# Performance work log

Measured on AMD Instinct MI355X. Metric: run time of the kernel, lower is better.

## Reference

```python
import jax, jax.numpy as jnp
from jax import lax
import numpy as np

CLASS_NUMBER = 19
REGION_RADIUS = 1
KERNEL = 2 * REGION_RADIUS + 1  # 3
IMAGE_TOPK = 256
EPS = 1e-6


def setup_inputs() -> dict:
    key = jax.random.key(0)
    # softmax-like probabilities over classes
    raw = jax.random.uniform(key, (4, CLASS_NUMBER, 512, 1024), dtype=jnp.float32)
    logit = raw / jnp.sum(raw, axis=1, keepdims=True)
    return {"logit": logit}


def _box_sum(x):
    # kxk box sum with zero padding (SAME for odd kernel == pad=radius)
    return lax.reduce_window(x, jnp.float32(0), lax.add,
                             (1, 1, KERNEL, KERNEL), (1, 1, 1, 1), 'SAME')


def reference(logit):
    B, C, H, W = logit.shape
    logC = jnp.log(jnp.float32(C))

    # region uncertainty: normalized entropy, then avg-pool (count_include_pad)
    entropy = jnp.sum(-logit * jnp.log(logit + EPS), axis=1, keepdims=True) / logC
    region_uncertainty = _box_sum(entropy) / (KERNEL * KERNEL)  # [B,1,H,W]

    # region impurity: argmax -> one-hot -> depthwise box-sum (ones kernel)
    predict = jnp.argmax(logit, axis=1)                       # [B,H,W]
    one_hot = jax.nn.one_hot(predict, C, axis=1, dtype=logit.dtype)  # [B,C,H,W]
    summary = _box_sum(one_hot)                               # [B,C,H,W]
    count = jnp.sum(summary, axis=1, keepdims=True)           # [B,1,H,W]
    dist = summary / count
    region_impurity = jnp.sum(-dist * jnp.log(dist + EPS), axis=1, keepdims=True) / logC

    score = region_uncertainty * region_impurity              # [B,1,H,W]

    # per-image score: sum of top-k region scores
    flat = score.reshape(B, H * W)
    topk_vals, _ = lax.top_k(flat, IMAGE_TOPK)
    image_score = jnp.sum(topk_vals, axis=1)                  # [B]
    return image_score
```

## Files before the change

### kernel.cpp

```cpp
#include <hip/hip_runtime.h>
#include <cstdint>
#include <cstddef>

#define BB 4
#define CC 19
#define HH 512
#define WW 1024
#define HW (HH*WW)
#define HW4 (HW/4)
#define BHW (BB*HW)
#define KTOP 256
#define EPSF 1e-6f
#define NB1 4096
#define NB2 8192
#define SEG 128
#define LSTRIDE 1032
#define LOGC 2.9444389791664403f

__device__ __forceinline__ unsigned int sortable(float x) {
    unsigned int u = __float_as_uint(x);
    return (u & 0x80000000u) ? ~u : (u | 0x80000000u);
}
__device__ __forceinline__ float unsortable(unsigned int K) {
    unsigned int u = (K & 0x80000000u) ? (K & 0x7FFFFFFFu) : ~K;
    return __uint_as_float(u);
}

__global__ __launch_bounds__(256) void k_ent(const float4* __restrict__ logit,
                                             float4* __restrict__ ent,
                                             uchar4* __restrict__ pred,
                                             unsigned int* __restrict__ histz,
                                             float* __restrict__ outz) {
    int idx = blockIdx.x * 256 + threadIdx.x;
    if (idx < 81928) histz[idx] = 0;
    if (idx < BB) outz[idx] = 0.f;
    int b = idx >> 17;
    int q = idx & (HW4 - 1);
    const float4* base = logit + (size_t)b * CC * HW4 + q;
    float e0 = 0.f, e1 = 0.f, e2 = 0.f, e3 = 0.f;
    float m0 = -1.f, m1 = -1.f, m2 = -1.f, m3 = -1.f;
    int a0 = 0, a1 = 0, a2 = 0, a3 = 0;
#pragma unroll
    for (int c = 0; c < CC; ++c) {
        float4 p = base[(size_t)c * HW4];
        e0 -= p.x * __logf(p.x + EPSF); if (p.x > m0) { m0 = p.x; a0 = c; }
        e1 -= p.y * __logf(p.y + EPSF); if (p.y > m1) { m1 = p.y; a1 = c; }
        e2 -= p.z * __logf(p.z + EPSF); if (p.z > m2) { m2 = p.z; a2 = c; }
        e3 -= p.w * __logf(p.w + EPSF); if (p.w > m3) { m3 = p.w; a3 = c; }
    }
    ent[idx] = make_float4(e0, e1, e2, e3);
    pred[idx] = make_uchar4((unsigned char)a0, (unsigned char)a1,
                            (unsigned char)a2, (unsigned char)a3);
}

__global__ __launch_bounds__(256) void k_score_hist(const float* __restrict__ ent,
                                                    const unsigned char* __restrict__ pred,
                                                    float* __restrict__ score,
                                                    unsigned int* __restrict__ hist1) {
    __shared__ __align__(16) float ent_s[6 * LSTRIDE];
    __shared__ __align__(16) unsigned char pred_s[6 * LSTRIDE];
    __shared__ unsigned int lh[NB1];
    __shared__ float lgt[48];
    int tid = threadIdx.x;
    int b = blockIdx.x >> 7;
    int seg = blockIdx.x & (SEG - 1);
    int r0 = seg * 4;

    for (int i = tid; i < 6 * LSTRIDE; i += 256) { ent_s[i] = 0.f; pred_s[i] = 255; }
    for (int i = tid; i < NB1; i += 256) lh[i] = 0;
    if (tid < 48) {
        int nvi = tid >> 4, cnt = tid & 15;
        float nv = (nvi == 0) ? 4.f : (nvi == 1) ? 6.f : 9.f;
        lgt[tid] = __logf((float)cnt / nv + EPSF);
    }
    __syncthreads();

    const float* eb = ent + (size_t)b * HW;
    const unsigned char* pb = pred + (size_t)b * HW;
    for (int i = tid; i < 1536; i += 256) {
        int rr = i >> 8, c4 = i & 255;
        int g = r0 - 1 + rr;
        if (g >= 0 && g < HH) {
            float4 v = *(const float4*)(eb + g * WW + c4 * 4);
            *(float4*)&ent_s[rr * LSTRIDE + 4 + c4 * 4] = v;
            uchar4 pv = *(const uchar4*)(pb + g * WW + c4 * 4);
            *(uchar4*)&pred_s[rr * LSTRIDE + 4 + c4 * 4] = pv;
        }
    }
    __syncthreads();

    float* sbuf = score + (size_t)b * HW;
#pragma unroll
    for (int it = 0; it < 16; ++it) {
        int p = it * 256 + tid;
        int py = p >> 10, px = p & 1023;
        int h = r0 + py, w = px;
        int l0 = py * LSTRIDE + 3 + px;
        float es = 0.f;
        int cls[9];
#pragma unroll
        for (int i = 0; i < 9; ++i) {
            int o = l0 + (i / 3) * LSTRIDE + (i % 3);
            es += ent_s[o];
            cls[i] = pred_s[o];
        }
        int nv = ((h > 0) + (h < HH - 1) + 1) * ((w > 0) + (w < WW - 1) + 1);
        float inv = 1.f / (float)nv;
        int nvi = (nv == 9) ? 2 : ((nv == 6) ? 1 : 0);
        const float* lg = &lgt[nvi * 16];
        float lsum = 0.f;
#pragma unroll
        for (int i = 0; i < 9; ++i) {
            int cnt = 0;
#pragma unroll
            for (int j = 0; j < 9; ++j) cnt += (cls[j] == cls[i]) ? 1 : 0;
            float lv = lg[cnt];
            lsum += (cls[i] != 255) ? lv : 0.f;
        }
        float imp = -inv * lsum;
        float v = (es * (1.f / (9.f * LOGC))) * (imp * (1.f / LOGC));
        sbuf[h * WW + w] = v;
        atomicAdd(&lh[sortable(v) >> 20], 1u);
    }
    __syncthreads();
    unsigned int* hb = hist1 + (size_t)b * NB1;
    for (int i = tid; i < NB1; i += 256) {
        unsigned int c = lh[i];
        if (c) atomicAdd(&hb[i], c);
    }
}

__device__ __forceinline__ void select4k(const unsigned int* __restrict__ hb,
                                         int rem, int* bin_out, int* rem_out) {
    __shared__ unsigned int cs[256];
    __shared__ unsigned int bs[16];
    __shared__ int s_chunk, s_bin, s_rem;
    int t = threadIdx.x;
    unsigned int s = 0;
#pragma unroll
    for (int i = 0; i < 16; ++i) s += hb[t * 16 + i];
    cs[t] = s;
    __syncthreads();
    for (int d = 1; d < 256; d <<= 1) {
        unsigned int v = (t + d < 256) ? cs[t + d] : 0;
        __syncthreads();
        cs[t] += v;
        __syncthreads();
    }
    unsigned int St = cs[t];
    unsigned int St1 = (t < 255) ? cs[t + 1] : 0;
    if ((int)St >= rem && (t == 255 || (int)St1 < rem)) {
        s_chunk = t; s_rem = rem - (int)St1;
    }
    __syncthreads();
    int chunk = s_chunk, rem2 = s_rem;
    if (t < 16) bs[t] = hb[chunk * 16 + t];
    __syncthreads();
    for (int d = 1; d < 16; d <<= 1) {
        unsigned int v = (t < 16 && t + d < 16) ? bs[t + d] : 0;
        __syncthreads();
        if (t < 16) bs[t] += v;
        __syncthreads();
    }
    if (t < 16) {
        unsigned int Sb = bs[t];
        unsigned int Sb1 = (t < 15) ? bs[t + 1] : 0;
        if ((int)Sb >= rem2 && (t == 15 || (int)Sb1 < rem2)) {
            s_bin = chunk * 16 + t; s_rem = rem2 - (int)Sb1;
        }
    }
    __syncthreads();
    *bin_out = s_bin;
    *rem_out = s_rem;
}

__device__ __forceinline__ void select8k(const unsigned int* __restrict__ hb,
                                         int rem, int* bin_out, int* rem_out) {
    __shared__ unsigned int cs[256];
    __shared__ unsigned int bs[32];
    __shared__ int s_chunk, s_bin, s_rem;
    int t = threadIdx.x;
    unsigned int s = 0;
#pragma unroll 8
    for (int i = 0; i < 32; ++i) s += hb[t * 32 + i];
    cs[t] = s;
    __syncthreads();
    for (int d = 1; d < 256; d <<= 1) {
        unsigned int v = (t + d < 256) ? cs[t + d] : 0;
        __syncthreads();
        cs[t] += v;
        __syncthreads();
    }
    unsigned int St = cs[t];
    unsigned int St1 = (t < 255) ? cs[t + 1] : 0;
    if ((int)St >= rem && (t == 255 || (int)St1 < rem)) {
        s_chunk = t; s_rem = rem - (int)St1;
    }
    __syncthreads();
    int chunk = s_chunk, rem2 = s_rem;
    if (t < 32) bs[t] = hb[chunk * 32 + t];
    __syncthreads();
    for (int d = 1; d < 32; d <<= 1) {
        unsigned int v = (t < 32 && t + d < 32) ? bs[t + d] : 0;
        __syncthreads();
        if (t < 32) bs[t] += v;
        __syncthreads();
    }
    if (t < 32) {
        unsigned int Sb = bs[t];
        unsigned int Sb1 = (t < 31) ? bs[t + 1] : 0;
        if ((int)Sb >= rem2 && (t == 31 || (int)Sb1 < rem2)) {
            s_bin = chunk * 32 + t; s_rem = rem2 - (int)Sb1;
        }
    }
    __syncthreads();
    *bin_out = s_bin;
    *rem_out = s_rem;
}

__global__ __launch_bounds__(256) void k_hist2(const float4* __restrict__ score,
                                               const unsigned int* __restrict__ hist1,
                                               unsigned int* __restrict__ hist2,
                                               float* __restrict__ hsum,
                                               unsigned int* __restrict__ T1g,
                                               int* __restrict__ r1g,
                                               float* __restrict__ out) {
    __shared__ unsigned int lh[NB2];
    __shared__ float ls[NB2];
    __shared__ float red[4];
    int b = blockIdx.x >> 7;
    int seg = blockIdx.x & (SEG - 1);
    int bin1, rem1;
    select4k(hist1 + (size_t)b * NB1, KTOP, &bin1, &rem1);
    unsigned int t1 = (unsigned int)bin1;
    if (seg == 0 && threadIdx.x == 0) { T1g[b] = t1; r1g[b] = rem1; }
    for (int i = threadIdx.x; i < NB2; i += 256) { lh[i] = 0; ls[i] = 0.f; }
    __syncthreads();
    const float4* p = score + ((size_t)b * HW + (size_t)seg * (HW / SEG)) / 4;
    float sa = 0.f;
    for (int i = threadIdx.x; i < (HW / SEG) / 4; i += 256) {
        float4 v = p[i];
        float vv[4] = {v.x, v.y, v.z, v.w};
#pragma unroll
        for (int q = 0; q < 4; ++q) {
            unsigned int k = sortable(vv[q]);
            unsigned int cb = k >> 20;
            if (cb > t1) sa += vv[q];
            else if (cb == t1) {
                int sub = (k >> 7) & 0x1FFF;
                atomicAdd(&lh[sub], 1u);
                atomicAdd(&ls[sub], vv[q]);
            }
        }
    }
    __syncthreads();
    unsigned int* hb = hist2 + (size_t)b * NB2;
    float* sb = hsum + (size_t)b * NB2;
    for (int i = threadIdx.x; i < NB2; i += 256) {
        unsigned int c = lh[i];
        if (c) { atomicAdd(&hb[i], c); atomicAdd(&sb[i], ls[i]); }
    }
#pragma unroll
    for (int d = 32; d; d >>= 1) sa += __shfl_down(sa, d);
    if ((threadIdx.x & 63) == 0) red[threadIdx.x >> 6] = sa;
    __syncthreads();
    if (threadIdx.x == 0) {
        float tt = red[0] + red[1] + red[2] + red[3];
        if (tt != 0.f) atomicAdd(&out[b], tt);
    }
}

__global__ __launch_bounds__(256) void k_scan2(const unsigned int* __restrict__ hist2,
                                               const float* __restrict__ hsum,
                                               const unsigned int* __restrict__ T1g,
                                               const int* __restrict__ r1g,
                                               float* __restrict__ out) {
    int b = blockIdx.x;
    int bin, rem;
    select8k(hist2 + (size_t)b * NB2, r1g[b], &bin, &rem);
    __shared__ float rs[256];
    int t = threadIdx.x;
    const float* sb = hsum + (size_t)b * NB2;
    float s = 0.f;
    for (int i = t; i < NB2; i += 256) if (i > bin) s += sb[i];
    rs[t] = s;
    __syncthreads();
    for (int d = 128; d; d >>= 1) {
        if (t < d) rs[t] += rs[t + d];
        __syncthreads();
    }
    if (t == 0) {
        unsigned int K = (T1g[b] << 20) | ((unsigned int)bin << 7);
        out[b] += rs[0] + unsortable(K) * (float)rem;
    }
}

extern "C" void kernel_launch(void* const* d_in, const int* in_sizes, int n_in,
                              void* d_out, int out_size, void* d_ws, size_t ws_size,
                              hipStream_t stream) {
    const float* logit = (const float*)d_in[0];
    float* out = (float*)d_out;
    char* ws = (char*)d_ws;

    float*         ent   = (float*)(ws);
    unsigned char* pred  = (unsigned char*)(ws + 8388608);
    float*         score = (float*)(ws + 10485760);
    unsigned int*  histb = (unsigned int*)(ws + 18874368);
    unsigned int*  hist1 = histb;
    unsigned int*  hist2 = histb + 16384;
    float*         hsum  = (float*)(histb + 49152);
    unsigned int*  T1g   = histb + 81920;
    int*           r1g   = (int*)(histb + 81924);

    k_ent<<<BHW / 4 / 256, 256, 0, stream>>>((const float4*)logit, (float4*)ent,
                                             (uchar4*)pred, histb, out);
    k_score_hist<<<BB * SEG, 256, 0, stream>>>(ent, pred, score, hist1);
    k_hist2<<<BB * SEG, 256, 0, stream>>>((const float4*)score, hist1,
                                          hist2, hsum, T1g, r1g, out);
    k_scan2<<<BB, 256, 0, stream>>>(hist2, hsum, T1g, r1g, out);
}
```

Baseline: 289.9 us.

## Fuse entropy and score kernels with neighbor-flag halo exchange, fold final scan

Merges the entropy/argmax pass and the 3x3 score/histogram pass into one kernel of 256 blocks with 1024 threads, each handling 8 rows. Entropy and prediction rows stay in shared memory, and only the boundary rows are written to global memory, so the full ent/pred round trip through HBM is avoided. Blocks exchange halo rows with their neighbors through agent-scope flags and spin-waits, which assumes all 256 blocks are co-resident and risks deadlock if they are not. The final scan kernel is folded into the histogram kernel using a last-block-done counter, which removes one launch.

```diff
diff --git a/kernel.cpp b/kernel.cpp
--- a/kernel.cpp
+++ b/kernel.cpp
@@ -8,14 +8,17 @@
 #define WW 1024
 #define HW (HH*WW)
 #define HW4 (HW/4)
-#define BHW (BB*HW)
 #define KTOP 256
 #define EPSF 1e-6f
 #define NB1 4096
 #define NB2 8192
-#define SEG 128
 #define LSTRIDE 1032
 #define LOGC 2.9444389791664403f
+
+#define NSEG 64
+#define RPB 8
+#define NBLK (BB*NSEG)
+#define SEGF 128
 
 __device__ __forceinline__ unsigned int sortable(float x) {
     unsigned int u = __float_as_uint(x);
@@ -25,108 +28,170 @@
     unsigned int u = (K & 0x80000000u) ? (K & 0x7FFFFFFFu) : ~K;
     return __uint_as_float(u);
 }
-
-__global__ __launch_bounds__(256) void k_ent(const float4* __restrict__ logit,
-                                             float4* __restrict__ ent,
-                                             uchar4* __restrict__ pred,
-                                             unsigned int* __restrict__ histz,
-                                             float* __restrict__ outz) {
-    int idx = blockIdx.x * 256 + threadIdx.x;
-    if (idx < 81928) histz[idx] = 0;
-    if (idx < BB) outz[idx] = 0.f;
-    int b = idx >> 17;
-    int q = idx & (HW4 - 1);
-    const float4* base = logit + (size_t)b * CC * HW4 + q;
-    float e0 = 0.f, e1 = 0.f, e2 = 0.f, e3 = 0.f;
-    float m0 = -1.f, m1 = -1.f, m2 = -1.f, m3 = -1.f;
-    int a0 = 0, a1 = 0, a2 = 0, a3 = 0;
-#pragma unroll
-    for (int c = 0; c < CC; ++c) {
-        float4 p = base[(size_t)c * HW4];
-        e0 -= p.x * __logf(p.x + EPSF); if (p.x > m0) { m0 = p.x; a0 = c; }
-        e1 -= p.y * __logf(p.y + EPSF); if (p.y > m1) { m1 = p.y; a1 = c; }
-        e2 -= p.z * __logf(p.z + EPSF); if (p.z > m2) { m2 = p.z; a2 = c; }
-        e3 -= p.w * __logf(p.w + EPSF); if (p.w > m3) { m3 = p.w; a3 = c; }
-    }
-    ent[idx] = make_float4(e0, e1, e2, e3);
-    pred[idx] = make_uchar4((unsigned char)a0, (unsigned char)a1,
-                            (unsigned char)a2, (unsigned char)a3);
-}
-
-__global__ __launch_bounds__(256) void k_score_hist(const float* __restrict__ ent,
-                                                    const unsigned char* __restrict__ pred,
-                                                    float* __restrict__ score,
-                                                    unsigned int* __restrict__ hist1) {
-    __shared__ __align__(16) float ent_s[6 * LSTRIDE];
-    __shared__ __align__(16) unsigned char pred_s[6 * LSTRIDE];
-    __shared__ unsigned int lh[NB1];
+__device__ __forceinline__ unsigned int agld(const unsigned int* p) {
+    return __hip_atomic_load(p, __ATOMIC_RELAXED, __HIP_MEMORY_SCOPE_AGENT);
+}
+__device__ __forceinline__ void agst(unsigned int* p, unsigned int v) {
+    __hip_atomic_store(p, v, __ATOMIC_RELAXED, __HIP_MEMORY_SCOPE_AGENT);
+}
+
+struct P1Mem {
+    float ent_s[(RPB + 2) * LSTRIDE];
+    unsigned char pred_s[(RPB + 2) * LSTRIDE];
+    unsigned int lh1[NB1];
+};
+union UMem { P1Mem p1; unsigned char pad[82000]; };
+
+__global__ __launch_bounds__(1024) void k_init(unsigned int* __restrict__ histb,
+                                               float* __restrict__ out) {
+    int i = blockIdx.x * 1024 + threadIdx.x;
+    if (i < 82180) histb[i] = 0u;
+    if (i < BB) out[i] = 0.f;
+}
+
+__global__ __launch_bounds__(1024, 4) void k_A(const float* __restrict__ logit,
+                                               float* __restrict__ ent,
+                                               unsigned char* __restrict__ pred,
+                                               float* __restrict__ score,
+                                               unsigned int* __restrict__ histb) {
+    __shared__ __align__(16) UMem U;
     __shared__ float lgt[48];
     int tid = threadIdx.x;
-    int b = blockIdx.x >> 7;
-    int seg = blockIdx.x & (SEG - 1);
-    int r0 = seg * 4;
-
-    for (int i = tid; i < 6 * LSTRIDE; i += 256) { ent_s[i] = 0.f; pred_s[i] = 255; }
-    for (int i = tid; i < NB1; i += 256) lh[i] = 0;
+    int tx = tid & 255;
+    int ty = tid >> 8;
+    int b = blockIdx.x >> 6;
+    int seg = blockIdx.x & (NSEG - 1);
+    int r0 = seg * RPB;
+
+    unsigned int* hist1 = histb;
+    unsigned int* flags = histb + 81920;
+
     if (tid < 48) {
         int nvi = tid >> 4, cnt = tid & 15;
         float nv = (nvi == 0) ? 4.f : (nvi == 1) ? 6.f : 9.f;
         lgt[tid] = __logf((float)cnt / nv + EPSF);
     }
-    __syncthreads();
-
-    const float* eb = ent + (size_t)b * HW;
-    const unsigned char* pb = pred + (size_t)b * HW;
-    for (int i = tid; i < 1536; i += 256) {
-        int rr = i >> 8, c4 = i & 255;
-        int g = r0 - 1 + rr;
+    for (int i = tid; i < (RPB + 2) * LSTRIDE; i += 1024) { U.p1.ent_s[i] = 0.f; U.p1.pred_s[i] = 255; }
+    for (int i = tid; i < NB1; i += 1024) U.p1.lh1[i] = 0;
+    __syncthreads();
+
+    {
+        const float4* bb4 = (const float4*)logit + (size_t)b * CC * HW4;
+#pragma unroll
+        for (int it = 0; it < 2; ++it) {
+            int lr = ty + it * 4;
+            int q = (r0 + lr) * 256 + tx;
+            const float4* basep = bb4 + q;
+            float e0 = 0.f, e1 = 0.f, e2 = 0.f, e3 = 0.f;
+            float m0 = -1.f, m1 = -1.f, m2 = -1.f, m3 = -1.f;
+            int a0 = 0, a1 = 0, a2 = 0, a3 = 0;
+#pragma unroll
+            for (int c = 0; c < CC; ++c) {
+                float4 p = basep[(size_t)c * HW4];
+                e0 -= p.x * __logf(p.x + EPSF); if (p.x > m0) { m0 = p.x; a0 = c; }
+                e1 -= p.y * __logf(p.y + EPSF); if (p.y > m1) { m1 = p.y; a1 = c; }
+                e2 -= p.z * __logf(p.z + EPSF); if (p.z > m2) { m2 = p.z; a2 = c; }
+                e3 -= p.w * __logf(p.w + EPSF); if (p.w > m3) { m3 = p.w; a3 = c; }
+            }
+            *(float4*)&U.p1.ent_s[(lr + 1) * LSTRIDE + 4 + tx * 4] = make_float4(e0, e1, e2, e3);
+            unsigned int pw = (unsigned int)a0 | ((unsigned int)a1 << 8) |
+                              ((unsigned int)a2 << 16) | ((unsigned int)a3 << 24);
+            *(unsigned int*)&U.p1.pred_s[(lr + 1) * LSTRIDE + 4 + tx * 4] = pw;
+            if (lr == 0 || lr == RPB - 1) {
+                unsigned int* ep = (unsigned int*)ent + (size_t)b * HW + (size_t)(r0 + lr) * WW + tx * 4;
+                agst(ep + 0, __float_as_uint(e0));
+                agst(ep + 1, __float_as_uint(e1));
+                agst(ep + 2, __float_as_uint(e2));
+                agst(ep + 3, __float_as_uint(e3));
+                agst((unsigned int*)pred + (size_t)b * HW4 + (size_t)(r0 + lr) * 256 + tx, pw);
+            }
+        }
+    }
+    __syncthreads();
+    if (tid == 0) agst(&flags[blockIdx.x], 1u);
+    if (tid == 64 && seg > 0)
+        while (agld(&flags[blockIdx.x - 1]) == 0u) __builtin_amdgcn_s_sleep(2);
+    if (tid == 128 && seg < NSEG - 1)
+        while (agld(&flags[blockIdx.x + 1]) == 0u) __builtin_amdgcn_s_sleep(2);
+    __syncthreads();
+
+    if (tid < 512) {
+        int top = tid >> 8;
+        int c4 = tid & 255;
+        int rr = top * (RPB + 1);
+        int g = r0 - 1 + top * (RPB + 1);
         if (g >= 0 && g < HH) {
-            float4 v = *(const float4*)(eb + g * WW + c4 * 4);
-            *(float4*)&ent_s[rr * LSTRIDE + 4 + c4 * 4] = v;
-            uchar4 pv = *(const uchar4*)(pb + g * WW + c4 * 4);
-            *(uchar4*)&pred_s[rr * LSTRIDE + 4 + c4 * 4] = pv;
+            const unsigned int* eu = (const unsigned int*)ent + (size_t)b * HW + (size_t)g * WW + c4 * 4;
+            float4 v;
+            v.x = __uint_as_float(agld(eu + 0));
+            v.y = __uint_as_float(agld(eu + 1));
+            v.z = __uint_as_float(agld(eu + 2));
+            v.w = __uint_as_float(agld(eu + 3));
+            *(float4*)&U.p1.ent_s[rr * LSTRIDE + 4 + c4 * 4] = v;
+            unsigned int pw = agld((const unsigned int*)pred + (size_t)b * HW4 + (size_t)g * 256 + c4);
+            *(unsigned int*)&U.p1.pred_s[rr * LSTRIDE + 4 + c4 * 4] = pw;
         }
     }
     __syncthreads();
 
     float* sbuf = score + (size_t)b * HW;
 #pragma unroll
-    for (int it = 0; it < 16; ++it) {
-        int p = it * 256 + tid;
-        int py = p >> 10, px = p & 1023;
-        int h = r0 + py, w = px;
-        int l0 = py * LSTRIDE + 3 + px;
-        float es = 0.f;
-        int cls[9];
-#pragma unroll
-        for (int i = 0; i < 9; ++i) {
-            int o = l0 + (i / 3) * LSTRIDE + (i % 3);
-            es += ent_s[o];
-            cls[i] = pred_s[o];
-        }
-        int nv = ((h > 0) + (h < HH - 1) + 1) * ((w > 0) + (w < WW - 1) + 1);
-        float inv = 1.f / (float)nv;
-        int nvi = (nv == 9) ? 2 : ((nv == 6) ? 1 : 0);
-        const float* lg = &lgt[nvi * 16];
-        float lsum = 0.f;
-#pragma unroll
-        for (int i = 0; i < 9; ++i) {
-            int cnt = 0;
-#pragma unroll
-            for (int j = 0; j < 9; ++j) cnt += (cls[j] == cls[i]) ? 1 : 0;
-            float lv = lg[cnt];
-            lsum += (cls[i] != 255) ? lv : 0.f;
-        }
-        float imp = -inv * lsum;
-        float v = (es * (1.f / (9.f * LOGC))) * (imp * (1.f / LOGC));
-        sbuf[h * WW + w] = v;
-        atomicAdd(&lh[sortable(v) >> 20], 1u);
-    }
-    __syncthreads();
-    unsigned int* hb = hist1 + (size_t)b * NB1;
-    for (int i = tid; i < NB1; i += 256) {
-        unsigned int c = lh[i];
-        if (c) atomicAdd(&hb[i], c);
+    for (int it = 0; it < 2; ++it) {
+        int k = ty + it * 4;
+        float r3[3][6];
+        int p3[3][6];
+#pragma unroll
+        for (int rr = 0; rr < 3; ++rr) {
+            const float* rowp = &U.p1.ent_s[(k + rr) * LSTRIDE + 4];
+            const unsigned char* prow = &U.p1.pred_s[(k + rr) * LSTRIDE + 4];
+            float4 m = *(const float4*)&rowp[tx * 4];
+            r3[rr][0] = rowp[tx * 4 - 1];
+            r3[rr][1] = m.x; r3[rr][2] = m.y; r3[rr][3] = m.z; r3[rr][4] = m.w;
+            r3[rr][5] = rowp[tx * 4 + 4];
+            uchar4 pm = *(const uchar4*)&prow[tx * 4];
+            p3[rr][0] = prow[tx * 4 - 1];
+            p3[rr][1] = pm.x; p3[rr][2] = pm.y; p3[rr][3] = pm.z; p3[rr][4] = pm.w;
+            p3[rr][5] = prow[tx * 4 + 4];
+        }
+        int h = r0 + k;
+        int hn = (h > 0) + (h < HH - 1) + 1;
+        float sv[4];
+#pragma unroll
+        for (int q = 0; q < 4; ++q) {
+            int w = tx * 4 + q;
+            float es = 0.f;
+#pragma unroll
+            for (int i = 0; i < 9; ++i) es += r3[i / 3][q + i % 3];
+            int cls[9];
+#pragma unroll
+            for (int i = 0; i < 9; ++i) cls[i] = p3[i / 3][q + i % 3];
+            int nv = hn * ((w > 0) + (w < WW - 1) + 1);
+            float inv = 1.f / (float)nv;
+            int nvi = (nv == 9) ? 2 : ((nv == 6) ? 1 : 0);
+            const float* lg = &lgt[nvi * 16];
+            float lsum = 0.f;
+#pragma unroll
+            for (int i = 0; i < 9; ++i) {
+                int cnt = 0;
+#pragma unroll
+                for (int j = 0; j < 9; ++j) cnt += (cls[j] == cls[i]) ? 1 : 0;
+                float lv = lg[cnt];
+                lsum += (cls[i] != 255) ? lv : 0.f;
+            }
+            float imp = -inv * lsum;
+            float v = (es * (1.f / (9.f * LOGC))) * (imp * (1.f / LOGC));
+            sv[q] = v;
+            atomicAdd(&U.p1.lh1[sortable(v) >> 20], 1u);
+        }
+        *(float4*)&sbuf[(size_t)h * WW + tx * 4] = make_float4(sv[0], sv[1], sv[2], sv[3]);
+    }
+    __syncthreads();
+    {
+        unsigned int* hb = hist1 + (size_t)b * NB1;
+        for (int i = tid; i < NB1; i += 1024) {
+            unsigned int c = U.p1.lh1[i];
+            if (c) atomicAdd(&hb[i], c);
+        }
     }
 }
 
@@ -174,15 +239,15 @@
     *rem_out = s_rem;
 }
 
-__device__ __forceinline__ void select8k(const unsigned int* __restrict__ hb,
-                                         int rem, int* bin_out, int* rem_out) {
+__device__ __forceinline__ void select8k_ag(const unsigned int* __restrict__ hb,
+                                            int rem, int* bin_out, int* rem_out) {
     __shared__ unsigned int cs[256];
     __shared__ unsigned int bs[32];
     __shared__ int s_chunk, s_bin, s_rem;
     int t = threadIdx.x;
     unsigned int s = 0;
 #pragma unroll 8
-    for (int i = 0; i < 32; ++i) s += hb[t * 32 + i];
+    for (int i = 0; i < 32; ++i) s += agld(&hb[t * 32 + i]);
     cs[t] = s;
     __syncthreads();
     for (int d = 1; d < 256; d <<= 1) {
@@ -198,7 +263,7 @@
     }
     __syncthreads();
     int chunk = s_chunk, rem2 = s_rem;
-    if (t < 32) bs[t] = hb[chunk * 32 + t];
+    if (t < 32) bs[t] = agld(&hb[chunk * 32 + t]);
     __syncthreads();
     for (int d = 1; d < 32; d <<= 1) {
         unsigned int v = (t < 32 && t + d < 32) ? bs[t + d] : 0;
@@ -218,27 +283,27 @@
     *rem_out = s_rem;
 }
 
-__global__ __launch_bounds__(256) void k_hist2(const float4* __restrict__ score,
-                                               const unsigned int* __restrict__ hist1,
-                                               unsigned int* __restrict__ hist2,
-                                               float* __restrict__ hsum,
-                                               unsigned int* __restrict__ T1g,
-                                               int* __restrict__ r1g,
-                                               float* __restrict__ out) {
+__global__ __launch_bounds__(256) void k_B(const float4* __restrict__ score,
+                                           const unsigned int* __restrict__ hist1,
+                                           unsigned int* __restrict__ hist2,
+                                           float* __restrict__ hsum,
+                                           unsigned int* __restrict__ done,
+                                           float* __restrict__ out) {
     __shared__ unsigned int lh[NB2];
     __shared__ float ls[NB2];
     __shared__ float red[4];
+    __shared__ float rs[256];
+    __shared__ int islast;
     int b = blockIdx.x >> 7;
-    int seg = blockIdx.x & (SEG - 1);
+    int seg = blockIdx.x & (SEGF - 1);
     int bin1, rem1;
     select4k(hist1 + (size_t)b * NB1, KTOP, &bin1, &rem1);
     unsigned int t1 = (unsigned int)bin1;
-    if (seg == 0 && threadIdx.x == 0) { T1g[b] = t1; r1g[b] = rem1; }
     for (int i = threadIdx.x; i < NB2; i += 256) { lh[i] = 0; ls[i] = 0.f; }
     __syncthreads();
-    const float4* p = score + ((size_t)b * HW + (size_t)seg * (HW / SEG)) / 4;
+    const float4* p = score + ((size_t)b * HW + (size_t)seg * (HW / SEGF)) / 4;
     float sa = 0.f;
-    for (int i = threadIdx.x; i < (HW / SEG) / 4; i += 256) {
+    for (int i = threadIdx.x; i < (HW / SEGF) / 4; i += 256) {
         float4 v = p[i];
         float vv[4] = {v.x, v.y, v.z, v.w};
 #pragma unroll
@@ -254,11 +319,13 @@
         }
     }
     __syncthreads();
-    unsigned int* hb = hist2 + (size_t)b * NB2;
-    float* sb = hsum + (size_t)b * NB2;
-    for (int i = threadIdx.x; i < NB2; i += 256) {
-        unsigned int c = lh[i];
-        if (c) { atomicAdd(&hb[i], c); atomicAdd(&sb[i], ls[i]); }
+    {
+        unsigned int* hb = hist2 + (size_t)b * NB2;
+        float* sb = hsum + (size_t)b * NB2;
+        for (int i = threadIdx.x; i < NB2; i += 256) {
+            unsigned int c = lh[i];
+            if (c) { atomicAdd(&hb[i], c); atomicAdd(&sb[i], ls[i]); }
+        }
     }
 #pragma unroll
     for (int d = 32; d; d >>= 1) sa += __shfl_down(sa, d);
@@ -268,30 +335,30 @@
         float tt = red[0] + red[1] + red[2] + red[3];
         if (tt != 0.f) atomicAdd(&out[b], tt);
     }
-}
-
-__global__ __launch_bounds__(256) void k_scan2(const unsigned int* __restrict__ hist2,
-                                               const float* __restrict__ hsum,
-                                               const unsigned int* __restrict__ T1g,
-                                               const int* __restrict__ r1g,
-                                               float* __restrict__ out) {
-    int b = blockIdx.x;
-    int bin, rem;
-    select8k(hist2 + (size_t)b * NB2, r1g[b], &bin, &rem);
-    __shared__ float rs[256];
-    int t = threadIdx.x;
-    const float* sb = hsum + (size_t)b * NB2;
-    float s = 0.f;
-    for (int i = t; i < NB2; i += 256) if (i > bin) s += sb[i];
-    rs[t] = s;
-    __syncthreads();
-    for (int d = 128; d; d >>= 1) {
-        if (t < d) rs[t] += rs[t + d];
-        __syncthreads();
-    }
-    if (t == 0) {
-        unsigned int K = (T1g[b] << 20) | ((unsigned int)bin << 7);
-        out[b] += rs[0] + unsortable(K) * (float)rem;
+    __syncthreads();
+    if (threadIdx.x == 0) {
+        unsigned int prev = __hip_atomic_fetch_add(&done[b], 1u, __ATOMIC_RELAXED,
+                                                   __HIP_MEMORY_SCOPE_AGENT);
+        islast = (prev == (unsigned int)(SEGF - 1)) ? 1 : 0;
+    }
+    __syncthreads();
+    if (islast) {
+        int bin, rem;
+        select8k_ag(hist2 + (size_t)b * NB2, rem1, &bin, &rem);
+        const unsigned int* sb = (const unsigned int*)(hsum + (size_t)b * NB2);
+        float s = 0.f;
+        for (int i = threadIdx.x; i < NB2; i += 256)
+            if (i > bin) s += __uint_as_float(agld(&sb[i]));
+        rs[threadIdx.x] = s;
+        __syncthreads();
+        for (int d = 128; d; d >>= 1) {
+            if (threadIdx.x < d) rs[threadIdx.x] += rs[threadIdx.x + d];
+            __syncthreads();
+        }
+        if (threadIdx.x == 0) {
+            unsigned int K = (t1 << 20) | ((unsigned int)bin << 7);
+            atomicAdd(&out[b], rs[0] + unsortable(K) * (float)rem);
+        }
     }
 }
 
@@ -309,13 +376,9 @@
     unsigned int*  hist1 = histb;
     unsigned int*  hist2 = histb + 16384;
     float*         hsum  = (float*)(histb + 49152);
-    unsigned int*  T1g   = histb + 81920;
-    int*           r1g   = (int*)(histb + 81924);
-
-    k_ent<<<BHW / 4 / 256, 256, 0, stream>>>((const float4*)logit, (float4*)ent,
-                                             (uchar4*)pred, histb, out);
-    k_score_hist<<<BB * SEG, 256, 0, stream>>>(ent, pred, score, hist1);
-    k_hist2<<<BB * SEG, 256, 0, stream>>>((const float4*)score, hist1,
-                                          hist2, hsum, T1g, r1g, out);
-    k_scan2<<<BB, 256, 0, stream>>>(hist2, hsum, T1g, r1g, out);
-}
+    unsigned int*  done  = histb + 82176;
+
+    k_init<<<81, 1024, 0, stream>>>(histb, out);
+    k_A<<<NBLK, 1024, 0, stream>>>(logit, ent, pred, score, histb);
+    k_B<<<BB * SEGF, 256, 0, stream>>>((const float4*)score, hist1, hist2, hsum, done, out);
+}
```

Result: no change. 289.9 us (-0.0%).
